# Performance work log

Hardware: AMD Instinct MI355X
Metric: run time of the kernel (lower is better)

Reference implementation:

```python
import jax, jax.numpy as jnp
from jax import lax
import numpy as np

N, K, F, H, NG, T = 32768, 16, 64, 128, 1024, 2


def setup_inputs() -> dict:
    key = jax.random.key(0)
    ks = jax.random.split(key, 24)
    def rn(k, shape, s=0.05):
        return jax.random.normal(k, shape, jnp.float32) * s
    inp = {
        'n': jax.random.normal(ks[0], (N, F), jnp.float32),
        'nbr': jax.random.randint(ks[1], (N, K), 0, N),
        # deterministic sorted graph ids -> every graph non-empty (safe segment_max)
        'gid': (jnp.arange(N) * NG) // N,
        'G': NG,
        # SAGEConv layer 1: LSTM(F,F), fc_self/fc_neigh F->H
        'lstm1_Wih': rn(ks[2], (F, 4 * F)), 'lstm1_Whh': rn(ks[3], (F, 4 * F)), 'lstm1_b': jnp.zeros((4 * F,), jnp.float32),
        'fcs1_W': rn(ks[4], (F, H)), 'fcs1_b': jnp.zeros((H,), jnp.float32),
        'fcn1_W': rn(ks[5], (F, H)), 'fcn1_b': jnp.zeros((H,), jnp.float32),
        # SAGEConv layer 2: LSTM(H,H), fc_self/fc_neigh H->H
        'lstm2_Wih': rn(ks[6], (H, 4 * H)), 'lstm2_Whh': rn(ks[7], (H, 4 * H)), 'lstm2_b': jnp.zeros((4 * H,), jnp.float32),
        'fcs2_W': rn(ks[8], (H, H)), 'fcs2_b': jnp.zeros((H,), jnp.float32),
        'fcn2_W': rn(ks[9], (H, H)), 'fcn2_b': jnp.zeros((H,), jnp.float32),
        # WeightedSumAndMax atom weighting: H->1
        'rw_W': rn(ks[10], (H, 1)), 'rw_b': jnp.zeros((1,), jnp.float32),
        # task head: 2H->H, H->T
        'h1_W': rn(ks[11], (2 * H, H)), 'h1_b': jnp.zeros((H,), jnp.float32),
        'h2_W': rn(ks[12], (H, T)), 'h2_b': jnp.zeros((T,), jnp.float32),
    }
    return inp


def _lstm_last(xseq, Wih, Whh, b):
    # xseq: [N, K, Fin]; returns last hidden state [N, Hh]
    Hh = Whh.shape[0]
    h0 = jnp.zeros((xseq.shape[0], Hh), xseq.dtype)
    def step(carry, xt):
        h, c = carry
        g = xt @ Wih + h @ Whh + b  # [N, 4H], torch gate order i,f,g,o
        i, f, gg, o = jnp.split(g, 4, axis=-1)
        c = jax.nn.sigmoid(f) * c + jax.nn.sigmoid(i) * jnp.tanh(gg)
        h = jax.nn.sigmoid(o) * jnp.tanh(c)
        return (h, c), None
    (h, _), _ = lax.scan(step, (h0, h0), jnp.swapaxes(xseq, 0, 1))
    return h


def _sage_layer(x, nbr, Wih, Whh, b, Ws, bs, Wn, bn):
    hn = _lstm_last(x[nbr], Wih, Whh, b)          # LSTM aggregate of neighbors
    return jax.nn.sigmoid(x @ Ws + bs + hn @ Wn + bn)


def reference(n, nbr, gid, G,
              lstm1_Wih, lstm1_Whh, lstm1_b, fcs1_W, fcs1_b, fcn1_W, fcn1_b,
              lstm2_Wih, lstm2_Whh, lstm2_b, fcs2_W, fcs2_b, fcn2_W, fcn2_b,
              rw_W, rw_b, h1_W, h1_b, h2_W, h2_b):
    G = int(G)
    h1 = _sage_layer(n, nbr, lstm1_Wih, lstm1_Whh, lstm1_b, fcs1_W, fcs1_b, fcn1_W, fcn1_b)
    h2 = _sage_layer(h1, nbr, lstm2_Wih, lstm2_Whh, lstm2_b, fcs2_W, fcs2_b, fcn2_W, fcn2_b)
    # WeightedSumAndMax readout
    w = jax.nn.sigmoid(h2 @ rw_W + rw_b)                       # [N,1]
    wsum = jax.ops.segment_sum(w * h2, gid, num_segments=G)    # [G,H]
    mx = jax.ops.segment_max(h2, gid, num_segments=G)          # [G,H]
    gemb = jnp.concatenate([wsum, mx], axis=-1)                # [G,2H]
    y = jax.nn.sigmoid(gemb @ h1_W + h1_b)
    y = jax.nn.sigmoid(y @ h2_W + h2_b)                        # classification
    return y
```

## Files before the change

### kernel.cpp

```cpp
#include <hip/hip_runtime.h>

typedef unsigned short u16;
typedef __attribute__((ext_vector_type(8))) short bf16x8;
typedef __attribute__((ext_vector_type(4))) float f32x4;
typedef __attribute__((ext_vector_type(2))) float f32x2;

constexpr int N_ = 32768;
constexpr int H_ = 128;
constexpr int G_ = 1024;
constexpr int T_ = 2;

__device__ __forceinline__ float sigf(float x){
  float e = __builtin_amdgcn_exp2f(x * -1.44269504f);
  return __builtin_amdgcn_rcpf(1.0f + e);
}
__device__ __forceinline__ f32x2 sig2(f32x2 x){
  f32x2 t = x * -1.44269504f;
  f32x2 e; e.x = __builtin_amdgcn_exp2f(t.x); e.y = __builtin_amdgcn_exp2f(t.y);
  f32x2 d = e + 1.0f;
  f32x2 r; r.x = __builtin_amdgcn_rcpf(d.x); r.y = __builtin_amdgcn_rcpf(d.y);
  return r;
}
__device__ __forceinline__ f32x2 tanh2(f32x2 x){
  f32x2 t = x * 2.88539008f;
  f32x2 e; e.x = __builtin_amdgcn_exp2f(t.x); e.y = __builtin_amdgcn_exp2f(t.y);
  f32x2 d = e + 1.0f;
  f32x2 r; r.x = __builtin_amdgcn_rcpf(d.x); r.y = __builtin_amdgcn_rcpf(d.y);
  return 1.0f - 2.0f*r;
}
__device__ __forceinline__ u16 f2bf(float f){
  unsigned u = __float_as_uint(f);
  unsigned r = (u + 0x7FFFu + ((u>>16)&1u))>>16;
  return (u16)r;
}
__device__ __forceinline__ unsigned cvt_pk_bf16(float a, float b){
  unsigned r;
  asm("v_cvt_pk_bf16_f32 %0, %1, %2" : "=v"(r) : "v"(a), "v"(b));
  return r;
}
__device__ __forceinline__ float bf2f(u16 h){ return __uint_as_float(((unsigned)h)<<16); }
__device__ __forceinline__ float asf(unsigned u){ return __uint_as_float(u); }
__device__ __forceinline__ f32x4 mfma16(bf16x8 a, bf16x8 b, f32x4 c){
  return __builtin_amdgcn_mfma_f32_16x16x32_bf16(a,b,c,0,0,0);
}

__global__ void pack_kernel(const float* __restrict__ src, int srcNC,
                            u16* __restrict__ dst, int NTtot, int ntOff, int ntCnt,
                            int Fh, int permMode)
{
  const int ntl  = blockIdx.x % ntCnt;
  const int kt   = blockIdx.x / ntCnt;
  const int lane = threadIdx.x;
  const int n = lane & 15, qq = lane >> 4;
  int pr = ntl*16 + n;
  int o;
  if (permMode == 1)      o = ((pr>>4)&3)*Fh + ((pr>>6)<<4) + (pr&15);
  else if (permMode == 2) o = (pr&3)*Fh + ((pr>>6)<<4) + ((pr>>2)&15);
  else                    o = pr;
  u16* d = dst + ((size_t)((kt*NTtot + ntOff + ntl)*64 + lane))*8;
#pragma unroll
  for (int j = 0; j < 8; ++j) {
    int k = kt*32 + qq*8 + j;
    d[j] = f2bf(src[(size_t)k*srcNC + o]);
  }
}

__global__ void biaspack_kernel(const float* __restrict__ b1, const float* __restrict__ bs1,
                                const float* __restrict__ bn1,
                                const float* __restrict__ b2, const float* __restrict__ bs2,
                                const float* __restrict__ bn2,
                                u16* __restrict__ bY1, u16* __restrict__ bY2)
{
  int tid = threadIdx.x;
  if (tid < 384) {
    int p = tid; float v;
    if (p < 256) { int o = (p&3)*64 + ((p>>6)<<4) + ((p>>2)&15); v = b1[o]; }
    else         { int j = p-256; v = bs1[j] + bn1[j]; }
    bY1[p] = f2bf(v);
  } else {
    int p = tid - 384; float v;
    if (p < 512) { int o = (p&3)*128 + ((p>>6)<<4) + ((p>>2)&15); v = b2[o]; }
    else         { int j = p-512; v = bs2[j] + bn2[j]; }
    bY2[p] = f2bf(v);
  }
}

template<int KT, int NTT, int AF32, int MODE>
__global__ __launch_bounds__(256, 2)
void gemm_kernel(const void* __restrict__ Ain,
                 const u16* __restrict__ Bpk,
                 const u16* __restrict__ biasbf,
                 const u16* __restrict__ Sp, int s_stride, int s_coloff,
                 u16* __restrict__ out, int out_stride)
{
  constexpr int KA  = KT*32;
  constexpr int NTW = NTT/4;
  constexpr int STR = KA + 8;
  static_assert(NTT % 4 == 0, "");
  __shared__ __align__(16) u16 a_lds[32*STR];
  const int tid  = threadIdx.x;
  const int base = blockIdx.x*32;
  {
    const int sub = tid & 7, rowl = tid >> 3;
    if constexpr (AF32) {
      const float* src = (const float*)Ain + (size_t)(base+rowl)*KA;
#pragma unroll
      for (int cc = 0; cc < KA/32; ++cc) {
        int e0 = (cc*8+sub)*4;
        float4 v = *(const float4*)(src + e0);
        ushort4 b;
        b.x = f2bf(v.x); b.y = f2bf(v.y); b.z = f2bf(v.z); b.w = f2bf(v.w);
        *(ushort4*)(void*)(a_lds + rowl*STR + e0) = b;
      }
    } else {
      const u16* src = (const u16*)Ain + (size_t)(base+rowl)*KA;
#pragma unroll
      for (int cc = 0; cc < KA/64; ++cc) {
        int e0 = (cc*8+sub)*8;
        uint4 v = *(const uint4*)(const void*)(src + e0);
        *(uint4*)(void*)(a_lds + rowl*STR + e0) = v;
      }
    }
  }
  __syncthreads();
  const int lane = tid & 63, w = tid >> 6;
  const int lc = lane & 15, q = lane >> 4;
  f32x4 acc[2][NTW];
  f32x4 z = {0.f,0.f,0.f,0.f};
#pragma unroll
  for (int m = 0; m < 2; ++m)
#pragma unroll
    for (int j = 0; j < NTW; ++j) acc[m][j] = z;
#pragma unroll
  for (int kt = 0; kt < KT; ++kt) {
    bf16x8 af0 = *(const bf16x8*)(const void*)(a_lds + lc*STR      + kt*32 + q*8);
    bf16x8 af1 = *(const bf16x8*)(const void*)(a_lds + (lc+16)*STR + kt*32 + q*8);
#pragma unroll
    for (int j = 0; j < NTW; ++j) {
      bf16x8 bf = *(const bf16x8*)(const void*)(Bpk + ((size_t)((kt*NTT + w*NTW + j)*64 + lane))*8);
      acc[0][j] = mfma16(af0, bf, acc[0][j]);
      acc[1][j] = mfma16(af1, bf, acc[1][j]);
    }
  }
#pragma unroll
  for (int m = 0; m < 2; ++m)
#pragma unroll
    for (int j = 0; j < NTW; ++j) {
      int col = (w*NTW + j)*16 + lc;
#pragma unroll
      for (int r = 0; r < 4; ++r) {
        int row = base + m*16 + q*4 + r;
        float v = acc[m][j][r];
        if constexpr (MODE == 0) {
          v += bf2f(biasbf[col]);
        } else {
          v += bf2f(Sp[(size_t)row*s_stride + s_coloff + col]);
          v = sigf(v);
        }
        out[(size_t)row*out_stride + col] = f2bf(v);
      }
    }
}

template<int KT>
__global__ __launch_bounds__(KT*128, 4)
void lstm_kernel(const int* __restrict__ nbr,
                 const u16* __restrict__ Y, int nctot,
                 const u16* __restrict__ Bpk,
                 u16* __restrict__ hK)
{
  constexpr int F   = KT*32;
  constexpr int NW  = KT*2;
  constexpr int NTT = KT*8;
  constexpr int STR = F + 8;
  __shared__ __align__(16) u16 h_lds[2][32*STR];
  __shared__ int nbr_s[32*16];
  const int tid  = threadIdx.x;
  const int base = blockIdx.x*32;
  const int lane = tid & 63, w = tid >> 6;
  const int lc = lane & 15, q = lane >> 4;

  for (int i = tid; i < 512; i += NW*64) nbr_s[i] = nbr[base*16 + i];

  bf16x8 bfr[KT][4];
#pragma unroll
  for (int kt = 0; kt < KT; ++kt)
#pragma unroll
    for (int g = 0; g < 4; ++g)
      bfr[kt][g] = *(const bf16x8*)(const void*)(Bpk + ((size_t)((kt*NTT + w*4 + g)*64 + lane))*8);

  f32x2 cs[2][2];
#pragma unroll
  for (int m = 0; m < 2; ++m)
#pragma unroll
    for (int rp = 0; rp < 2; ++rp) cs[m][rp] = (f32x2){0.f, 0.f};
  __syncthreads();

  const u16* Yb = Y + (size_t)(w*64 + lc*4);
  const int wcol = w*16 + lc;
  for (int t = 0; t < 16; ++t) {
    const u16* hr = h_lds[t & 1];
    u16*       hw = h_lds[(t & 1) ^ 1];
    uint2 yv[2][4];
#pragma unroll
    for (int m = 0; m < 2; ++m)
#pragma unroll
      for (int r = 0; r < 4; ++r) {
        int vr = nbr_s[(m*16 + q*4 + r)*16 + t];
        yv[m][r] = *(const uint2*)(const void*)(Yb + (size_t)vr*nctot);
      }
#pragma unroll
    for (int m = 0; m < 2; ++m) {
      f32x4 acc[4];
      f32x4 z = {0.f,0.f,0.f,0.f};
#pragma unroll
      for (int g = 0; g < 4; ++g) acc[g] = z;
      if (t != 0) {
#pragma unroll
        for (int kt = 0; kt < KT; ++kt) {
          bf16x8 af = *(const bf16x8*)(const void*)(hr + (lc + m*16)*STR + kt*32 + q*8);
#pragma unroll
          for (int g = 0; g < 4; ++g) acc[g] = mfma16(af, bfr[kt][g], acc[g]);
        }
      }
#pragma unroll
      for (int rp = 0; rp < 2; ++rp) {
        uint2 ya = yv[m][2*rp], yb = yv[m][2*rp+1];
        f32x2 yi = { asf(ya.x<<16),          asf(yb.x<<16) };
        f32x2 yf = { asf(ya.x&0xffff0000u),  asf(yb.x&0xffff0000u) };
        f32x2 yg = { asf(ya.y<<16),          asf(yb.y<<16) };
        f32x2 yo = { asf(ya.y&0xffff0000u),  asf(yb.y&0xffff0000u) };
        f32x2 gi = (f32x2){acc[0][2*rp], acc[0][2*rp+1]} + yi;
        f32x2 gf = (f32x2){acc[1][2*rp], acc[1][2*rp+1]} + yf;
        f32x2 gg = (f32x2){acc[2][2*rp], acc[2][2*rp+1]} + yg;
        f32x2 go = (f32x2){acc[3][2*rp], acc[3][2*rp+1]} + yo;
        f32x2 c  = sig2(gf)*cs[m][rp] + sig2(gi)*tanh2(gg);
        cs[m][rp] = c;
        f32x2 hh = sig2(go)*tanh2(c);
        unsigned pkd = cvt_pk_bf16(hh.x, hh.y);
        int r0 = m*16 + q*4 + 2*rp;
        hw[r0*STR + wcol]     = (u16)pkd;
        hw[(r0+1)*STR + wcol] = (u16)(pkd >> 16);
      }
    }
    __syncthreads();
  }
  const u16* hf = h_lds[0];
  for (int i = tid; i < 32*F; i += NW*64) {
    int row = i / F, col = i % F;
    hK[(size_t)base*F + i] = hf[row*STR + col];
  }
}

__global__ __launch_bounds__(128)
void head_kernel(const u16* __restrict__ h2, const float* __restrict__ rwW,
                 const float* __restrict__ rwb,
                 const float* __restrict__ h1W, const float* __restrict__ h1b,
                 const float* __restrict__ h2W, const float* __restrict__ h2b,
                 float* __restrict__ out)
{
  __shared__ float h2s[32*H_];
  __shared__ float part[32*4];
  __shared__ float wv[32];
  __shared__ float gemb[2*H_];
  __shared__ float y1[H_];
  const int g = blockIdx.x, t = threadIdx.x;
  for (int r = 0; r < 32; ++r)
    h2s[r*H_ + t] = bf2f(h2[(size_t)(g*32 + r)*H_ + t]);
  __syncthreads();
  { int r = t>>2, qq = t&3; float p = 0.f;
    for (int h = qq*32; h < qq*32+32; ++h) p += h2s[r*H_+h]*rwW[h];
    part[r*4+qq] = p; }
  __syncthreads();
  if (t < 32) wv[t] = sigf(part[t*4]+part[t*4+1]+part[t*4+2]+part[t*4+3]+rwb[0]);
  __syncthreads();
  { float wsum=0.f, mx=-3.402823466e38f;
    for (int r = 0; r < 32; ++r) { float v = h2s[r*H_+t]; wsum += wv[r]*v; mx = fmaxf(mx,v); }
    gemb[t]=wsum; gemb[H_+t]=mx; }
  __syncthreads();
  { float a = h1b[t];
    for (int k = 0; k < 2*H_; ++k) a += gemb[k]*h1W[k*H_+t];
    y1[t]=sigf(a); }
  __syncthreads();
  if (t < T_) {
    float a = h2b[t];
    for (int h = 0; h < H_; ++h) a += y1[h]*h2W[h*T_+t];
    out[(size_t)g*T_+t] = sigf(a);
  }
}

extern "C" void kernel_launch(void* const* d_in, const int* in_sizes, int n_in,
                              void* d_out, int out_size, void* d_ws, size_t ws_size,
                              hipStream_t stream) {
  const float* n_feat = (const float*)d_in[0];
  const int*   nbr    = (const int*)d_in[1];
  const float* l1Wih = (const float*)d_in[4];
  const float* l1Whh = (const float*)d_in[5];
  const float* l1b   = (const float*)d_in[6];
  const float* fcs1W = (const float*)d_in[7];
  const float* fcs1b = (const float*)d_in[8];
  const float* fcn1W = (const float*)d_in[9];
  const float* fcn1b = (const float*)d_in[10];
  const float* l2Wih = (const float*)d_in[11];
  const float* l2Whh = (const float*)d_in[12];
  const float* l2b   = (const float*)d_in[13];
  const float* fcs2W = (const float*)d_in[14];
  const float* fcs2b = (const float*)d_in[15];
  const float* fcn2W = (const float*)d_in[16];
  const float* fcn2b = (const float*)d_in[17];
  const float* rwW   = (const float*)d_in[18];
  const float* rwb   = (const float*)d_in[19];
  const float* h1W   = (const float*)d_in[20];
  const float* h1b   = (const float*)d_in[21];
  const float* h2W   = (const float*)d_in[22];
  const float* h2b   = (const float*)d_in[23];

  char* ws = (char*)d_ws;
  u16* Y   = (u16*)(ws);
  u16* h1  = (u16*)(ws + 41943040);
  u16* hK1 = (u16*)(ws + 50331648);
  u16* h2  = (u16*)(ws + 54525952);
  char* wt = ws + 62914560;
  u16* BY1 = (u16*)(wt);
  u16* BW1 = (u16*)(wt + 49152);
  u16* BN1 = (u16*)(wt + 81920);
  u16* BY2 = (u16*)(wt + 98304);
  u16* BW2 = (u16*)(wt + 262144);
  u16* BN2 = (u16*)(wt + 393216);
  u16* bY1 = (u16*)(wt + 425984);
  u16* bY2 = (u16*)(wt + 427008);
  u16* hK2 = h1;

  pack_kernel<<<32, 64, 0, stream>>>(l1Wih, 256, BY1, 24, 0, 16, 64, 2);
  pack_kernel<<<16, 64, 0, stream>>>(fcs1W, 128, BY1, 24, 16, 8, 0, 0);
  pack_kernel<<<32, 64, 0, stream>>>(l1Whh, 256, BW1, 16, 0, 16, 64, 1);
  pack_kernel<<<16, 64, 0, stream>>>(fcn1W, 128, BN1, 8, 0, 8, 0, 0);
  pack_kernel<<<128, 64, 0, stream>>>(l2Wih, 512, BY2, 40, 0, 32, 128, 2);
  pack_kernel<<<32, 64, 0, stream>>>(fcs2W, 128, BY2, 40, 32, 8, 0, 0);
  pack_kernel<<<128, 64, 0, stream>>>(l2Whh, 512, BW2, 32, 0, 32, 128, 1);
  pack_kernel<<<32, 64, 0, stream>>>(fcn2W, 128, BN2, 8, 0, 8, 0, 0);
  biaspack_kernel<<<1, 1024, 0, stream>>>(l1b, fcs1b, fcn1b, l2b, fcs2b, fcn2b, bY1, bY2);

  gemm_kernel<2,24,1,0><<<1024, 256, 0, stream>>>(n_feat, BY1, bY1, nullptr, 0, 0, Y, 384);
  lstm_kernel<2><<<1024, 256, 0, stream>>>(nbr, Y, 384, BW1, hK1);
  gemm_kernel<2,8,0,1><<<1024, 256, 0, stream>>>(hK1, BN1, nullptr, Y, 384, 256, h1, 128);

  gemm_kernel<4,40,0,0><<<1024, 256, 0, stream>>>(h1, BY2, bY2, nullptr, 0, 0, Y, 640);
  lstm_kernel<4><<<1024, 512, 0, stream>>>(nbr, Y, 640, BW2, hK2);
  gemm_kernel<4,8,0,1><<<1024, 256, 0, stream>>>(hK2, BN2, nullptr, Y, 640, 512, h2, 128);

  head_kernel<<<G_, 128, 0, stream>>>(h2, rwW, rwb, h1W, h1b, h2W, h2b, (float*)d_out);
}
```

Baseline: 343.7 us.

## Fuse neighbor FC into LSTM epilogue, prefetch gathers, merge pack kernels

The fc_neigh GEMM plus sigmoid is folded into the end of the LSTM kernel, which consumes the final hidden state directly from LDS. This removes the hK round trip through global memory and two kernel launches. The neighbor-row gathers for step t+1 are now issued after step t's compute, so their latency overlaps the barrier and the next MFMA work. The nine weight and bias pack launches are merged into a single kernel. The cost is higher register pressure in the LSTM kernel from the extra prefetch buffers and epilogue accumulators.

```diff
diff --git a/kernel.cpp b/kernel.cpp
--- a/kernel.cpp
+++ b/kernel.cpp
@@ -44,19 +44,52 @@
   return __builtin_amdgcn_mfma_f32_16x16x32_bf16(a,b,c,0,0,0);
 }
 
-__global__ void pack_kernel(const float* __restrict__ src, int srcNC,
-                            u16* __restrict__ dst, int NTtot, int ntOff, int ntCnt,
-                            int Fh, int permMode)
+__global__ __launch_bounds__(64)
+void pack_all(const float* __restrict__ l1Wih, const float* __restrict__ fcs1W,
+              const float* __restrict__ l1Whh, const float* __restrict__ fcn1W,
+              const float* __restrict__ l2Wih, const float* __restrict__ fcs2W,
+              const float* __restrict__ l2Whh, const float* __restrict__ fcn2W,
+              const float* __restrict__ l1b, const float* __restrict__ bs1,
+              const float* __restrict__ bn1,
+              const float* __restrict__ l2b, const float* __restrict__ bs2,
+              const float* __restrict__ bn2,
+              u16* BY1, u16* BW1, u16* BN1, u16* BY2, u16* BW2, u16* BN2,
+              u16* bY1, u16* bY2)
 {
-  const int ntl  = blockIdx.x % ntCnt;
-  const int kt   = blockIdx.x / ntCnt;
+  int b = blockIdx.x;
   const int lane = threadIdx.x;
+  if (b == 416) {
+    for (int i = lane; i < 1024; i += 64) {
+      if (i < 384) {
+        int p = i; float v;
+        if (p < 256) { int o = (p&3)*64 + ((p>>6)<<4) + ((p>>2)&15); v = l1b[o]; }
+        else         { int j = p-256; v = bs1[j] + bn1[j]; }
+        bY1[p] = f2bf(v);
+      } else {
+        int p = i - 384; float v;
+        if (p < 512) { int o = (p&3)*128 + ((p>>6)<<4) + ((p>>2)&15); v = l2b[o]; }
+        else         { int j = p-512; v = bs2[j] + bn2[j]; }
+        bY2[p] = f2bf(v);
+      }
+    }
+    return;
+  }
+  const float* src; u16* dst; int srcNC, NTtot, ntOff, ntCnt, Fh, perm;
+  if      (b < 32)  { src=l1Wih; dst=BY1; srcNC=256; NTtot=24; ntOff=0;  ntCnt=16; Fh=64;  perm=2; }
+  else if (b < 48)  { src=fcs1W; dst=BY1; srcNC=128; NTtot=24; ntOff=16; ntCnt=8;  Fh=0;   perm=0; b-=32; }
+  else if (b < 80)  { src=l1Whh; dst=BW1; srcNC=256; NTtot=16; ntOff=0;  ntCnt=16; Fh=64;  perm=1; b-=48; }
+  else if (b < 96)  { src=fcn1W; dst=BN1; srcNC=128; NTtot=8;  ntOff=0;  ntCnt=8;  Fh=0;   perm=0; b-=80; }
+  else if (b < 224) { src=l2Wih; dst=BY2; srcNC=512; NTtot=40; ntOff=0;  ntCnt=32; Fh=128; perm=2; b-=96; }
+  else if (b < 256) { src=fcs2W; dst=BY2; srcNC=128; NTtot=40; ntOff=32; ntCnt=8;  Fh=0;   perm=0; b-=224; }
+  else if (b < 384) { src=l2Whh; dst=BW2; srcNC=512; NTtot=32; ntOff=0;  ntCnt=32; Fh=128; perm=1; b-=256; }
+  else              { src=fcn2W; dst=BN2; srcNC=128; NTtot=8;  ntOff=0;  ntCnt=8;  Fh=0;   perm=0; b-=384; }
+  const int ntl = b % ntCnt, kt = b / ntCnt;
   const int n = lane & 15, qq = lane >> 4;
   int pr = ntl*16 + n;
   int o;
-  if (permMode == 1)      o = ((pr>>4)&3)*Fh + ((pr>>6)<<4) + (pr&15);
-  else if (permMode == 2) o = (pr&3)*Fh + ((pr>>6)<<4) + ((pr>>2)&15);
-  else                    o = pr;
+  if (perm == 1)      o = ((pr>>4)&3)*Fh + ((pr>>6)<<4) + (pr&15);
+  else if (perm == 2) o = (pr&3)*Fh + ((pr>>6)<<4) + ((pr>>2)&15);
+  else                o = pr;
   u16* d = dst + ((size_t)((kt*NTtot + ntOff + ntl)*64 + lane))*8;
 #pragma unroll
   for (int j = 0; j < 8; ++j) {
@@ -65,38 +98,16 @@
   }
 }
 
-__global__ void biaspack_kernel(const float* __restrict__ b1, const float* __restrict__ bs1,
-                                const float* __restrict__ bn1,
-                                const float* __restrict__ b2, const float* __restrict__ bs2,
-                                const float* __restrict__ bn2,
-                                u16* __restrict__ bY1, u16* __restrict__ bY2)
-{
-  int tid = threadIdx.x;
-  if (tid < 384) {
-    int p = tid; float v;
-    if (p < 256) { int o = (p&3)*64 + ((p>>6)<<4) + ((p>>2)&15); v = b1[o]; }
-    else         { int j = p-256; v = bs1[j] + bn1[j]; }
-    bY1[p] = f2bf(v);
-  } else {
-    int p = tid - 384; float v;
-    if (p < 512) { int o = (p&3)*128 + ((p>>6)<<4) + ((p>>2)&15); v = b2[o]; }
-    else         { int j = p-512; v = bs2[j] + bn2[j]; }
-    bY2[p] = f2bf(v);
-  }
-}
-
-template<int KT, int NTT, int AF32, int MODE>
+template<int KT, int NTT, int AF32>
 __global__ __launch_bounds__(256, 2)
 void gemm_kernel(const void* __restrict__ Ain,
                  const u16* __restrict__ Bpk,
                  const u16* __restrict__ biasbf,
-                 const u16* __restrict__ Sp, int s_stride, int s_coloff,
                  u16* __restrict__ out, int out_stride)
 {
   constexpr int KA  = KT*32;
   constexpr int NTW = NTT/4;
   constexpr int STR = KA + 8;
-  static_assert(NTT % 4 == 0, "");
   __shared__ __align__(16) u16 a_lds[32*STR];
   const int tid  = threadIdx.x;
   const int base = blockIdx.x*32;
@@ -108,9 +119,9 @@
       for (int cc = 0; cc < KA/32; ++cc) {
         int e0 = (cc*8+sub)*4;
         float4 v = *(const float4*)(src + e0);
-        ushort4 b;
-        b.x = f2bf(v.x); b.y = f2bf(v.y); b.z = f2bf(v.z); b.w = f2bf(v.w);
-        *(ushort4*)(void*)(a_lds + rowl*STR + e0) = b;
+        ushort4 bv;
+        bv.x = f2bf(v.x); bv.y = f2bf(v.y); bv.z = f2bf(v.z); bv.w = f2bf(v.w);
+        *(ushort4*)(void*)(a_lds + rowl*STR + e0) = bv;
       }
     } else {
       const u16* src = (const u16*)Ain + (size_t)(base+rowl)*KA;
@@ -150,14 +161,7 @@
 #pragma unroll
       for (int r = 0; r < 4; ++r) {
         int row = base + m*16 + q*4 + r;
-        float v = acc[m][j][r];
-        if constexpr (MODE == 0) {
-          v += bf2f(biasbf[col]);
-        } else {
-          v += bf2f(Sp[(size_t)row*s_stride + s_coloff + col]);
-          v = sigf(v);
-        }
-        out[(size_t)row*out_stride + col] = f2bf(v);
+        out[(size_t)row*out_stride + col] = f2bf(acc[m][j][r] + bf2f(biasbf[col]));
       }
     }
 }
@@ -167,14 +171,16 @@
 void lstm_kernel(const int* __restrict__ nbr,
                  const u16* __restrict__ Y, int nctot,
                  const u16* __restrict__ Bpk,
-                 u16* __restrict__ hK)
+                 const u16* __restrict__ BN,
+                 const u16* __restrict__ Sp, int s_stride, int s_coloff,
+                 u16* __restrict__ out)
 {
   constexpr int F   = KT*32;
   constexpr int NW  = KT*2;
   constexpr int NTT = KT*8;
   constexpr int STR = F + 8;
   __shared__ __align__(16) u16 h_lds[2][32*STR];
-  __shared__ int nbr_s[32*16];
+  __shared__ int nbr_s[512];
   const int tid  = threadIdx.x;
   const int base = blockIdx.x*32;
   const int lane = tid & 63, w = tid >> 6;
@@ -196,19 +202,23 @@
     for (int rp = 0; rp < 2; ++rp) cs[m][rp] = (f32x2){0.f, 0.f};
   __syncthreads();
 
-  const u16* Yb = Y + (size_t)(w*64 + lc*4);
+  const char* Yb = (const char*)Y;
+  const unsigned rowbytes = (unsigned)nctot * 2u;
+  const unsigned lanebyte = (unsigned)(w*64 + lc*4) * 2u;
   const int wcol = w*16 + lc;
+
+  uint2 yv[2][4];
+#pragma unroll
+  for (int m = 0; m < 2; ++m)
+#pragma unroll
+    for (int r = 0; r < 4; ++r) {
+      unsigned vr = (unsigned)nbr_s[(m*16 + q*4 + r)*16 + 0];
+      yv[m][r] = *(const uint2*)(const void*)(Yb + (vr*rowbytes + lanebyte));
+    }
+
   for (int t = 0; t < 16; ++t) {
     const u16* hr = h_lds[t & 1];
     u16*       hw = h_lds[(t & 1) ^ 1];
-    uint2 yv[2][4];
-#pragma unroll
-    for (int m = 0; m < 2; ++m)
-#pragma unroll
-      for (int r = 0; r < 4; ++r) {
-        int vr = nbr_s[(m*16 + q*4 + r)*16 + t];
-        yv[m][r] = *(const uint2*)(const void*)(Yb + (size_t)vr*nctot);
-      }
 #pragma unroll
     for (int m = 0; m < 2; ++m) {
       f32x4 acc[4];
@@ -243,12 +253,44 @@
         hw[(r0+1)*STR + wcol] = (u16)(pkd >> 16);
       }
     }
+    if (t < 15) {
+#pragma unroll
+      for (int m = 0; m < 2; ++m)
+#pragma unroll
+        for (int r = 0; r < 4; ++r) {
+          unsigned vr = (unsigned)nbr_s[(m*16 + q*4 + r)*16 + t + 1];
+          yv[m][r] = *(const uint2*)(const void*)(Yb + (vr*rowbytes + lanebyte));
+        }
+    }
     __syncthreads();
   }
+
+  constexpr int CPW = 8 / NW;
   const u16* hf = h_lds[0];
-  for (int i = tid; i < 32*F; i += NW*64) {
-    int row = i / F, col = i % F;
-    hK[(size_t)base*F + i] = hf[row*STR + col];
+#pragma unroll
+  for (int cc2 = 0; cc2 < CPW; ++cc2) {
+    const int nt = w*CPW + cc2;
+    f32x4 a2[2];
+    f32x4 z = {0.f,0.f,0.f,0.f};
+    a2[0] = z; a2[1] = z;
+#pragma unroll
+    for (int kt = 0; kt < KT; ++kt) {
+      bf16x8 nf = *(const bf16x8*)(const void*)(BN + ((size_t)((kt*8 + nt)*64 + lane))*8);
+#pragma unroll
+      for (int m = 0; m < 2; ++m) {
+        bf16x8 af = *(const bf16x8*)(const void*)(hf + (lc + m*16)*STR + kt*32 + q*8);
+        a2[m] = mfma16(af, nf, a2[m]);
+      }
+    }
+    const int col = nt*16 + lc;
+#pragma unroll
+    for (int m = 0; m < 2; ++m)
+#pragma unroll
+      for (int r = 0; r < 4; ++r) {
+        int row = base + m*16 + q*4 + r;
+        float v = a2[m][r] + bf2f(Sp[(size_t)row*s_stride + s_coloff + col]);
+        out[(size_t)row*H_ + col] = f2bf(sigf(v));
+      }
   }
 }
 
@@ -318,9 +360,8 @@
   char* ws = (char*)d_ws;
   u16* Y   = (u16*)(ws);
   u16* h1  = (u16*)(ws + 41943040);
-  u16* hK1 = (u16*)(ws + 50331648);
-  u16* h2  = (u16*)(ws + 54525952);
-  char* wt = ws + 62914560;
+  u16* h2  = (u16*)(ws + 50331648);
+  char* wt = ws + 58720256;
   u16* BY1 = (u16*)(wt);
   u16* BW1 = (u16*)(wt + 49152);
   u16* BN1 = (u16*)(wt + 81920);
@@ -328,26 +369,18 @@
   u16* BW2 = (u16*)(wt + 262144);
   u16* BN2 = (u16*)(wt + 393216);
   u16* bY1 = (u16*)(wt + 425984);
-  u16* bY2 = (u16*)(wt + 427008);
-  u16* hK2 = h1;
-
-  pack_kernel<<<32, 64, 0, stream>>>(l1Wih, 256, BY1, 24, 0, 16, 64, 2);
-  pack_kernel<<<16, 64, 0, stream>>>(fcs1W, 128, BY1, 24, 16, 8, 0, 0);
-  pack_kernel<<<32, 64, 0, stream>>>(l1Whh, 256, BW1, 16, 0, 16, 64, 1);
-  pack_kernel<<<16, 64, 0, stream>>>(fcn1W, 128, BN1, 8, 0, 8, 0, 0);
-  pack_kernel<<<128, 64, 0, stream>>>(l2Wih, 512, BY2, 40, 0, 32, 128, 2);
-  pack_kernel<<<32, 64, 0, stream>>>(fcs2W, 128, BY2, 40, 32, 8, 0, 0);
-  pack_kernel<<<128, 64, 0, stream>>>(l2Whh, 512, BW2, 32, 0, 32, 128, 1);
-  pack_kernel<<<32, 64, 0, stream>>>(fcn2W, 128, BN2, 8, 0, 8, 0, 0);
-  biaspack_kernel<<<1, 1024, 0, stream>>>(l1b, fcs1b, fcn1b, l2b, fcs2b, fcn2b, bY1, bY2);
-
-  gemm_kernel<2,24,1,0><<<1024, 256, 0, stream>>>(n_feat, BY1, bY1, nullptr, 0, 0, Y, 384);
-  lstm_kernel<2><<<1024, 256, 0, stream>>>(nbr, Y, 384, BW1, hK1);
-  gemm_kernel<2,8,0,1><<<1024, 256, 0, stream>>>(hK1, BN1, nullptr, Y, 384, 256, h1, 128);
-
-  gemm_kernel<4,40,0,0><<<1024, 256, 0, stream>>>(h1, BY2, bY2, nullptr, 0, 0, Y, 640);
-  lstm_kernel<4><<<1024, 512, 0, stream>>>(nbr, Y, 640, BW2, hK2);
-  gemm_kernel<4,8,0,1><<<1024, 256, 0, stream>>>(hK2, BN2, nullptr, Y, 640, 512, h2, 128);
+  u16* bY2 = (u16*)(wt + 426752);
+
+  pack_all<<<417, 64, 0, stream>>>(l1Wih, fcs1W, l1Whh, fcn1W,
+                                   l2Wih, fcs2W, l2Whh, fcn2W,
+                                   l1b, fcs1b, fcn1b, l2b, fcs2b, fcn2b,
+                                   BY1, BW1, BN1, BY2, BW2, BN2, bY1, bY2);
+
+  gemm_kernel<2,24,1><<<1024, 256, 0, stream>>>(n_feat, BY1, bY1, Y, 384);
+  lstm_kernel<2><<<1024, 256, 0, stream>>>(nbr, Y, 384, BW1, BN1, Y, 384, 256, h1);
+
+  gemm_kernel<4,40,0><<<1024, 256, 0, stream>>>(h1, BY2, bY2, Y, 640);
+  lstm_kernel<4><<<1024, 512, 0, stream>>>(nbr, Y, 640, BW2, BN2, Y, 640, 512, h2);
 
   head_kernel<<<G_, 128, 0, stream>>>(h2, rwW, rwb, h1W, h1b, h2W, h2b, (float*)d_out);
 }
```

New measurement: 311.7 us. 9.3% less time.
